# Kernel optimization log

Hardware: AMD Instinct MI355X
Metric: run time of the kernel (lower is better)

Reference implementation:

```python
import jax, jax.numpy as jnp
import numpy as np

MODEL_DIM = 512
INNER_DIM = 4 * MODEL_DIM
NUM_EXPERTS = 4
LN_EPS = 1e-5


def setup_inputs() -> dict:
    key = jax.random.key(0)
    ks = jax.random.split(key, 8)
    B, T, D, E = 8, 8192, MODEL_DIM, NUM_EXPERTS
    x = jax.random.normal(ks[0], (B, T, D), dtype=jnp.float32)
    router_prob = jax.random.uniform(ks[1], (B, T, E), dtype=jnp.float32)
    alpha = jnp.ones((), dtype=jnp.float32)
    # params (kaiming-uniform-ish init, values just need to be realistic)
    bound1 = 1.0 / np.sqrt(D)
    l1_w = jax.random.uniform(ks[2], (INNER_DIM, D), minval=-bound1, maxval=bound1, dtype=jnp.float32)
    l1_b = jax.random.uniform(ks[3], (INNER_DIM,), minval=-bound1, maxval=bound1, dtype=jnp.float32)
    bound2 = 1.0 / np.sqrt(INNER_DIM)
    l2_w = jax.random.uniform(ks[4], (D, INNER_DIM), minval=-bound2, maxval=bound2, dtype=jnp.float32)
    l2_b = jax.random.uniform(ks[5], (D,), minval=-bound2, maxval=bound2, dtype=jnp.float32)
    ln_w = jnp.ones((D,), dtype=jnp.float32)
    ln_b = jnp.zeros((D,), dtype=jnp.float32)
    return {"x": x, "router_prob": router_prob, "alpha": alpha,
            "ln_w": ln_w, "ln_b": ln_b,
            "l1_w": l1_w, "l1_b": l1_b, "l2_w": l2_w, "l2_b": l2_b}


def _layernorm(x, w, b):
    mu = jnp.mean(x, axis=-1, keepdims=True)
    var = jnp.var(x, axis=-1, keepdims=True)
    return (x - mu) * jax.lax.rsqrt(var + LN_EPS) * w + b


def reference(x, router_prob, alpha, ln_w, ln_b, l1_w, l1_b, l2_w, l2_b):
    B, T, D = x.shape
    E = router_prob.shape[-1]
    k = T // E
    brange = jnp.arange(B)[:, None]  # [B,1] for batched scatter
    rp = router_prob  # working copy; selected tokens get zeroed
    outs, probs = [], []
    for e in range(E):
        # top-k tokens for this expert among the not-yet-taken tokens
        _, idx = jax.lax.top_k(rp[:, :, e], k)          # idx: [B,k]
        xi = jnp.take_along_axis(x, idx[:, :, None], axis=1)            # [B,k,D]
        sp = jnp.take_along_axis(router_prob, idx[:, :, None], axis=1)  # [B,k,E]
        rp = rp.at[brange, idx, :].set(0.0)  # mark tokens as consumed
        # nested-width expert MLP
        xn = _layernorm(xi, ln_w, ln_b)
        m = D // (2 ** e)
        h = jax.nn.gelu(jnp.einsum('bkm,im->bki', xn[:, :, :m], l1_w[:, :m]) + l1_b,
                        approximate=False)                               # [B,k,INNER]
        o = jnp.einsum('bki,mi->bkm', h, l2_w[:m]) + l2_b[:m]            # [B,k,m]
        o = jnp.pad(o, ((0, 0), (0, 0), (0, D - m)))                     # pad back to D
        scale = alpha * sp[:, :, e:e + 1] + 1.0                          # [B,k,1]
        outs.append(xi + scale * o)
        probs.append(sp)
    final_outs = jnp.concatenate(outs, axis=1)   # [B,T,D]
    final_probs = jnp.concatenate(probs, axis=1) # [B,T,E]
    return final_outs, final_probs
```

## Files before the change

### kernel.cpp

```cpp
#include <hip/hip_runtime.h>
#include <hip/hip_bf16.h>

typedef __attribute__((ext_vector_type(8))) short  bf16x8;
typedef __attribute__((ext_vector_type(4))) short  s16x4;
typedef __attribute__((ext_vector_type(4))) float  f32x4;
typedef unsigned long long u64;

#define B_   8
#define T_   8192
#define D_   512
#define E_   4
#define INNER_ 2048
#define M_TOK 16384

static __device__ __forceinline__ short f2bf(float f) {
    union { float f; unsigned int u; } a; a.f = f;
    unsigned int u = a.u;
    u += 0x7FFFu + ((u >> 16) & 1u);
    return (short)(u >> 16);
}

static __device__ __forceinline__ void cswap(u64& a, u64& b, bool desc) {
    if (desc ? (a < b) : (a > b)) { u64 t = a; a = b; b = t; }
}

__global__ __launch_bounds__(256) void convertw(const float* __restrict__ w1,
                                                const float* __restrict__ w2,
                                                short* __restrict__ o1,
                                                short* __restrict__ o2) {
    int i = (blockIdx.x * 256 + threadIdx.x) * 4;
    if (i < 1048576) {
        float4 a = *(const float4*)(w1 + i);
        s16x4 ra; ra.x = f2bf(a.x); ra.y = f2bf(a.y); ra.z = f2bf(a.z); ra.w = f2bf(a.w);
        *(s16x4*)(o1 + i) = ra;
        float4 b = *(const float4*)(w2 + i);
        s16x4 rb; rb.x = f2bf(b.x); rb.y = f2bf(b.y); rb.z = f2bf(b.z); rb.w = f2bf(b.w);
        *(s16x4*)(o2 + i) = rb;
    }
}

__global__ __launch_bounds__(1024) void sort_kernel(const float* __restrict__ rp,
                                                    u64* __restrict__ sorted) {
    __shared__ u64 keys[8192];
    const int t = threadIdx.x;
    const int b = blockIdx.x >> 2, e = blockIdx.x & 3;
    const size_t base = (size_t)b * T_;

    u64 k[8];
    #pragma unroll
    for (int j = 0; j < 8; ++j) {
        int i = (t << 3) + j;
        float v = rp[(base + i) * E_ + e];
        unsigned vb; __builtin_memcpy(&vb, &v, 4);
        k[j] = (((u64)(vb + 1u)) << 13) | (u64)(8191 - i);
    }
    cswap(k[0], k[1], true);  cswap(k[2], k[3], false);
    cswap(k[4], k[5], true);  cswap(k[6], k[7], false);
    cswap(k[0], k[2], true);  cswap(k[1], k[3], true);
    cswap(k[4], k[6], false); cswap(k[5], k[7], false);
    cswap(k[0], k[1], true);  cswap(k[2], k[3], true);
    cswap(k[4], k[5], false); cswap(k[6], k[7], false);
    {
        bool d8 = ((t & 1) == 0);
        cswap(k[0], k[4], d8); cswap(k[1], k[5], d8); cswap(k[2], k[6], d8); cswap(k[3], k[7], d8);
        cswap(k[0], k[2], d8); cswap(k[1], k[3], d8); cswap(k[4], k[6], d8); cswap(k[5], k[7], d8);
        cswap(k[0], k[1], d8); cswap(k[2], k[3], d8); cswap(k[4], k[5], d8); cswap(k[6], k[7], d8);
    }
    #pragma unroll
    for (int j = 0; j < 8; ++j) keys[(t << 3) + j] = k[j];

    for (int size = 16; size <= 8192; size <<= 1) {
        for (int stride = size >> 1; stride >= 8; stride >>= 1) {
            __syncthreads();
            #pragma unroll
            for (int q = 0; q < 4; ++q) {
                int p = (q << 10) + t;
                int i = ((p & ~(stride - 1)) << 1) | (p & (stride - 1));
                int l = i | stride;
                bool desc = ((i & size) == 0);
                u64 a = keys[i], c = keys[l];
                if (desc ? (a < c) : (a > c)) { keys[i] = c; keys[l] = a; }
            }
        }
        __syncthreads();
        #pragma unroll
        for (int j = 0; j < 8; ++j) k[j] = keys[(t << 3) + j];
        bool d = (((t << 3) & size) == 0);
        cswap(k[0], k[4], d); cswap(k[1], k[5], d); cswap(k[2], k[6], d); cswap(k[3], k[7], d);
        cswap(k[0], k[2], d); cswap(k[1], k[3], d); cswap(k[4], k[6], d); cswap(k[5], k[7], d);
        cswap(k[0], k[1], d); cswap(k[2], k[3], d); cswap(k[4], k[5], d); cswap(k[6], k[7], d);
        #pragma unroll
        for (int j = 0; j < 8; ++j) keys[(t << 3) + j] = k[j];
    }
    __syncthreads();
    u64* dst = sorted + ((size_t)blockIdx.x << 13);
    #pragma unroll
    for (int j = 0; j < 8; ++j) {
        int i = (j << 10) + t;
        dst[i] = keys[i];
    }
}

__global__ __launch_bounds__(1024) void select_kernel(const float* __restrict__ rp,
                                                      const u64* __restrict__ sorted,
                                                      const float* __restrict__ alphaPtr,
                                                      int* __restrict__ perm,
                                                      float* __restrict__ scaleArr,
                                                      float* __restrict__ out_probs) {
    __shared__ unsigned char cons[8192];
    __shared__ int wsum[16];
    __shared__ int woff[16];
    const int t = threadIdx.x, b = blockIdx.x;
    const int lane = t & 63, wv = t >> 6;
    const size_t base = (size_t)b * T_;
    const float alphaV = *alphaPtr;

    #pragma unroll
    for (int j = 0; j < 8; ++j) cons[(t << 3) + j] = 0;
    __syncthreads();

    for (int e = 0; e < E_; ++e) {
        const u64* sk = sorted + (((size_t)(b << 2) + e) << 13);
        u64 k[8]; int idx[8]; int f[8];
        int s = 0;
        #pragma unroll
        for (int j = 0; j < 8; ++j) {
            k[j] = sk[(t << 3) + j];
            idx[j] = 8191 - (int)(k[j] & 8191ull);
            f[j] = cons[idx[j]] ? 0 : 1;
            s += f[j];
        }
        int inc = s;
        #pragma unroll
        for (int o = 1; o < 64; o <<= 1) {
            int v = __shfl_up(inc, o, 64);
            if (lane >= o) inc += v;
        }
        if (lane == 63) wsum[wv] = inc;
        __syncthreads();
        if (t == 0) {
            int acc = 0;
            for (int w = 0; w < 16; ++w) { int v = wsum[w]; woff[w] = acc; acc += v; }
        }
        __syncthreads();
        int off = woff[wv] + (inc - s);
        #pragma unroll
        for (int j = 0; j < 8; ++j) {
            if (f[j] && off < 2048) {
                int rank = off;
                unsigned vb = (unsigned)(k[j] >> 13) - 1u;
                float v; __builtin_memcpy(&v, &vb, 4);
                int rpos = (e << 14) + (b << 11) + rank;
                perm[rpos] = idx[j];
                scaleArr[rpos] = alphaV * v + 1.0f;
                size_t g = ((size_t)b << 13) + (e << 11) + rank;
                float4 pr = *(const float4*)(rp + ((base + idx[j]) << 2));
                *(float4*)(out_probs + (g << 2)) = pr;
                cons[idx[j]] = 1;
            }
            off += f[j];
        }
        __syncthreads();
    }
}

__global__ __launch_bounds__(256) void gather_ln(const float* __restrict__ x,
                                                 const int* __restrict__ perm,
                                                 const float* __restrict__ ln_w,
                                                 const float* __restrict__ ln_b,
                                                 short* __restrict__ xn,
                                                 float* __restrict__ out_outs) {
    const int wv = threadIdx.x >> 6, lane = threadIdx.x & 63;
    const int rp_ = (blockIdx.x << 2) + wv;
    const int e = rp_ >> 14, rem = rp_ & 16383, b = rem >> 11, rank = rem & 2047;
    const int idx = perm[rp_];
    const float* xr = x + (((size_t)b << 13) + idx) * D_;
    const int d0 = lane << 3;
    float4 v0 = *(const float4*)(xr + d0);
    float4 v1 = *(const float4*)(xr + d0 + 4);

    float s = v0.x + v0.y + v0.z + v0.w + v1.x + v1.y + v1.z + v1.w;
    #pragma unroll
    for (int o = 32; o > 0; o >>= 1) s += __shfl_xor(s, o, 64);
    float mu = s * (1.0f / 512.0f);

    float a0 = v0.x - mu, a1 = v0.y - mu, a2 = v0.z - mu, a3 = v0.w - mu;
    float a4 = v1.x - mu, a5 = v1.y - mu, a6 = v1.z - mu, a7 = v1.w - mu;
    float q = a0*a0 + a1*a1 + a2*a2 + a3*a3 + a4*a4 + a5*a5 + a6*a6 + a7*a7;
    #pragma unroll
    for (int o = 32; o > 0; o >>= 1) q += __shfl_xor(q, o, 64);
    float rstd = rsqrtf(q * (1.0f / 512.0f) + 1e-5f);

    const size_t g = ((size_t)b << 13) + (e << 11) + rank;
    float* op = out_outs + g * D_ + d0;
    *(float4*)op       = v0;
    *(float4*)(op + 4) = v1;

    float4 w0 = *(const float4*)(ln_w + d0);
    float4 w1 = *(const float4*)(ln_w + d0 + 4);
    float4 bb0 = *(const float4*)(ln_b + d0);
    float4 bb1 = *(const float4*)(ln_b + d0 + 4);
    bf16x8 hv;
    hv[0] = f2bf(a0 * rstd * w0.x + bb0.x);
    hv[1] = f2bf(a1 * rstd * w0.y + bb0.y);
    hv[2] = f2bf(a2 * rstd * w0.z + bb0.z);
    hv[3] = f2bf(a3 * rstd * w0.w + bb0.w);
    hv[4] = f2bf(a4 * rstd * w1.x + bb1.x);
    hv[5] = f2bf(a5 * rstd * w1.y + bb1.y);
    hv[6] = f2bf(a6 * rstd * w1.z + bb1.z);
    hv[7] = f2bf(a7 * rstd * w1.w + bb1.w);
    *(bf16x8*)(xn + (size_t)rp_ * D_ + d0) = hv;
}

template <int MODE>
__global__ __launch_bounds__(256) void gemm_bt(const short* __restrict__ A,
                                               const short* __restrict__ B,
                                               int N, int K, int lda, int ldb,
                                               const float* __restrict__ bias,
                                               short* __restrict__ H,
                                               float* __restrict__ Out,
                                               const float* __restrict__ scaleArr,
                                               int expert) {
    __shared__ short As[128 * 64];
    __shared__ short Bs[128 * 64];
    const int t = threadIdx.x;
    const int tile_n = blockIdx.x << 7;
    const int tile_m = blockIdx.y << 7;
    const int lane = t & 63, wave = t >> 6;
    const int wm = (wave >> 1) << 6, wn = (wave & 1) << 6;
    const int lrow = lane & 15, lk = (lane >> 4) << 3;
    const int ldsRow = lane >> 3;
    const int ldsCol = (lane & 7) << 3;

    f32x4 acc[4][4];
    #pragma unroll
    for (int i = 0; i < 4; ++i)
        #pragma unroll
        for (int j = 0; j < 4; ++j)
            acc[i][j] = (f32x4){0.f, 0.f, 0.f, 0.f};

    for (int k0 = 0; k0 < K; k0 += 64) {
        #pragma unroll
        for (int q = 0; q < 4; ++q) {
            int c = (wave << 2) + q;
            const short* ga = A + (size_t)(tile_m + (c << 3) + ldsRow) * lda + k0 + ldsCol;
            __builtin_amdgcn_global_load_lds(
                (const __attribute__((address_space(1))) unsigned int*)ga,
                (__attribute__((address_space(3))) unsigned int*)(As + (c << 9)),
                16, 0, 0);
            const short* gb = B + (size_t)(tile_n + (c << 3) + ldsRow) * ldb + k0 + ldsCol;
            __builtin_amdgcn_global_load_lds(
                (const __attribute__((address_space(1))) unsigned int*)gb,
                (__attribute__((address_space(3))) unsigned int*)(Bs + (c << 9)),
                16, 0, 0);
        }
        __syncthreads();
        bf16x8 af[4][2], bfr[4][2];
        #pragma unroll
        for (int f = 0; f < 4; ++f)
            #pragma unroll
            for (int kk = 0; kk < 2; ++kk) {
                af[f][kk]  = *(const bf16x8*)(As + ((wm + (f << 4) + lrow) << 6) + (kk << 5) + lk);
                bfr[f][kk] = *(const bf16x8*)(Bs + ((wn + (f << 4) + lrow) << 6) + (kk << 5) + lk);
            }
        #pragma unroll
        for (int kk = 0; kk < 2; ++kk)
            #pragma unroll
            for (int fm = 0; fm < 4; ++fm)
                #pragma unroll
                for (int fn = 0; fn < 4; ++fn)
                    acc[fm][fn] = __builtin_amdgcn_mfma_f32_16x16x32_bf16(
                        af[fm][kk], bfr[fn][kk], acc[fm][fn], 0, 0, 0);
        __syncthreads();
    }

    #pragma unroll
    for (int fm = 0; fm < 4; ++fm) {
        #pragma unroll
        for (int fn = 0; fn < 4; ++fn) {
            #pragma unroll
            for (int j = 0; j < 4; ++j) {
                int row = tile_m + wm + (fm << 4) + ((lane >> 4) << 2) + j;
                int col = tile_n + wn + (fn << 4) + (lane & 15);
                float v = acc[fm][fn][j];
                if (MODE == 1) {
                    v += bias[col];
                    v = 0.5f * v * (1.0f + erff(v * 0.7071067811865475f));
                    H[(size_t)row * (size_t)INNER_ + col] = f2bf(v);
                } else {
                    if (col < N) {
                        int bb = row >> 11, rank = row & 2047;
                        float sc = scaleArr[(expert << 14) + row];
                        float* p = Out + (((size_t)bb << 13) + (expert << 11) + rank) * D_ + col;
                        *p += sc * (v + bias[col]);
                    }
                }
            }
        }
    }
}

extern "C" void kernel_launch(void* const* d_in, const int* in_sizes, int n_in,
                              void* d_out, int out_size, void* d_ws, size_t ws_size,
                              hipStream_t stream) {
    const float* x           = (const float*)d_in[0];
    const float* router_prob = (const float*)d_in[1];
    const float* alpha       = (const float*)d_in[2];
    const float* ln_w        = (const float*)d_in[3];
    const float* ln_b        = (const float*)d_in[4];
    const float* l1_w        = (const float*)d_in[5];
    const float* l1_b        = (const float*)d_in[6];
    const float* l2_w        = (const float*)d_in[7];
    const float* l2_b        = (const float*)d_in[8];

    float* out       = (float*)d_out;
    float* out_probs = out + (size_t)B_ * T_ * D_;

    char* ws = (char*)d_ws;
    int*   perm  = (int*)(ws);
    float* scale = (float*)(ws + (1u << 18));
    short* w1b   = (short*)(ws + (2u << 18));
    short* w2b   = (short*)(ws + (2u << 18) + (1u << 21));
    short* xn    = (short*)(ws + (2u << 18) + (2u << 21));
    short* h     = (short*)(ws + (2u << 18) + (2u << 21) + (1u << 26));
    u64*   sorted = (u64*)h;

    convertw<<<1024, 256, 0, stream>>>(l1_w, l2_w, w1b, w2b);
    sort_kernel<<<32, 1024, 0, stream>>>(router_prob, sorted);
    select_kernel<<<8, 1024, 0, stream>>>(router_prob, sorted, alpha, perm, scale, out_probs);
    gather_ln<<<16384, 256, 0, stream>>>(x, perm, ln_w, ln_b, xn, out);

    for (int e = 0; e < E_; ++e) {
        int m = D_ >> e;
        gemm_bt<1><<<dim3(INNER_ / 128, M_TOK / 128), 256, 0, stream>>>(
            xn + ((size_t)e * M_TOK) * D_, w1b, INNER_, m, D_, D_, l1_b, h,
            nullptr, nullptr, 0);
        gemm_bt<2><<<dim3((m + 127) >> 7, M_TOK / 128), 256, 0, stream>>>(
            h, w2b, m, INNER_, INNER_, INNER_, l2_b, nullptr, out, scale, e);
    }
}
```

Measured before the change: 820.5 us.

## Batch expert GEMMs via grid z, split-K second GEMM, swizzle LDS, tanh GELU

After: 812.7 us. Within noise of the previous version (-0.9%).

```diff
diff --git a/kernel.cpp b/kernel.cpp
--- a/kernel.cpp
+++ b/kernel.cpp
@@ -215,22 +215,58 @@
 template <int MODE>
 __global__ __launch_bounds__(256) void gemm_bt(const short* __restrict__ A,
                                                const short* __restrict__ B,
-                                               int N, int K, int lda, int ldb,
+                                               int lda, int ldb,
                                                const float* __restrict__ bias,
                                                short* __restrict__ H,
                                                float* __restrict__ Out,
                                                const float* __restrict__ scaleArr,
-                                               int expert) {
+                                               int expertArg, size_t hStride) {
     __shared__ short As[128 * 64];
     __shared__ short Bs[128 * 64];
     const int t = threadIdx.x;
-    const int tile_n = blockIdx.x << 7;
+    const int lane = t & 63, wave = t >> 6;
+    const int e = expertArg + blockIdx.z;
     const int tile_m = blockIdx.y << 7;
-    const int lane = t & 63, wave = t >> 6;
+
+    int tile_n, kStart, nsteps, Ncols, sp;
+    bool useAtomic;
+    const short* Abase;
+    if (MODE == 1) {
+        tile_n = blockIdx.x << 7;
+        kStart = 0;
+        nsteps = (512 >> e) >> 6;
+        Ncols  = 2048;
+        Abase  = A + (size_t)e * M_TOK * D_;
+        sp = 0; useAtomic = false;
+    } else {
+        Ncols = 512 >> e;
+        int se = e < 2 ? e : 2;
+        int splits = 1 << se;
+        int sub = blockIdx.x;
+        int nt = sub >> se;
+        sp = sub & (splits - 1);
+        tile_n = nt << 7;
+        int Kslice = 2048 >> se;
+        kStart = sp * Kslice;
+        nsteps = Kslice >> 6;
+        Abase  = A + (size_t)e * hStride;
+        useAtomic = (splits > 1);
+    }
+
+    const int srow = lane >> 3;
+    const int scol = ((lane & 7) ^ srow) << 3;
+    const short* aP[4];
+    const short* bP[4];
+    #pragma unroll
+    for (int q = 0; q < 4; ++q) {
+        int c = (wave << 2) + q;
+        aP[q] = Abase + (size_t)(tile_m + (c << 3) + srow) * lda + kStart + scol;
+        bP[q] = B     + (size_t)(tile_n + (c << 3) + srow) * ldb + kStart + scol;
+    }
+
     const int wm = (wave >> 1) << 6, wn = (wave & 1) << 6;
-    const int lrow = lane & 15, lk = (lane >> 4) << 3;
-    const int ldsRow = lane >> 3;
-    const int ldsCol = (lane & 7) << 3;
+    const int lrow = lane & 15, lt = lane >> 4;
+    const int sx = lrow & 7;
 
     f32x4 acc[4][4];
     #pragma unroll
@@ -239,20 +275,19 @@
         for (int j = 0; j < 4; ++j)
             acc[i][j] = (f32x4){0.f, 0.f, 0.f, 0.f};
 
-    for (int k0 = 0; k0 < K; k0 += 64) {
+    for (int ks = 0; ks < nsteps; ++ks) {
         #pragma unroll
         for (int q = 0; q < 4; ++q) {
             int c = (wave << 2) + q;
-            const short* ga = A + (size_t)(tile_m + (c << 3) + ldsRow) * lda + k0 + ldsCol;
             __builtin_amdgcn_global_load_lds(
-                (const __attribute__((address_space(1))) unsigned int*)ga,
+                (const __attribute__((address_space(1))) unsigned int*)aP[q],
                 (__attribute__((address_space(3))) unsigned int*)(As + (c << 9)),
                 16, 0, 0);
-            const short* gb = B + (size_t)(tile_n + (c << 3) + ldsRow) * ldb + k0 + ldsCol;
             __builtin_amdgcn_global_load_lds(
-                (const __attribute__((address_space(1))) unsigned int*)gb,
+                (const __attribute__((address_space(1))) unsigned int*)bP[q],
                 (__attribute__((address_space(3))) unsigned int*)(Bs + (c << 9)),
                 16, 0, 0);
+            aP[q] += 64; bP[q] += 64;
         }
         __syncthreads();
         bf16x8 af[4][2], bfr[4][2];
@@ -260,8 +295,9 @@
         for (int f = 0; f < 4; ++f)
             #pragma unroll
             for (int kk = 0; kk < 2; ++kk) {
-                af[f][kk]  = *(const bf16x8*)(As + ((wm + (f << 4) + lrow) << 6) + (kk << 5) + lk);
-                bfr[f][kk] = *(const bf16x8*)(Bs + ((wn + (f << 4) + lrow) << 6) + (kk << 5) + lk);
+                int slot = (kk << 2) + lt;
+                af[f][kk]  = *(const bf16x8*)(As + ((wm + (f << 4) + lrow) << 6) + ((slot ^ sx) << 3));
+                bfr[f][kk] = *(const bf16x8*)(Bs + ((wn + (f << 4) + lrow) << 6) + ((slot ^ sx) << 3));
             }
         #pragma unroll
         for (int kk = 0; kk < 2; ++kk)
@@ -280,19 +316,24 @@
         for (int fn = 0; fn < 4; ++fn) {
             #pragma unroll
             for (int j = 0; j < 4; ++j) {
-                int row = tile_m + wm + (fm << 4) + ((lane >> 4) << 2) + j;
+                int row = tile_m + wm + (fm << 4) + (lt << 2) + j;
                 int col = tile_n + wn + (fn << 4) + (lane & 15);
                 float v = acc[fm][fn][j];
                 if (MODE == 1) {
                     v += bias[col];
-                    v = 0.5f * v * (1.0f + erff(v * 0.7071067811865475f));
-                    H[(size_t)row * (size_t)INNER_ + col] = f2bf(v);
+                    float u = 1.5957691216f * v * (1.0f + 0.044715f * v * v);
+                    u = fminf(u, 60.0f);
+                    float p = __expf(u);
+                    float g = v * p * __builtin_amdgcn_rcpf(p + 1.0f);
+                    (H + (size_t)e * hStride)[(size_t)row * (size_t)INNER_ + col] = f2bf(g);
                 } else {
-                    if (col < N) {
+                    if (col < Ncols) {
                         int bb = row >> 11, rank = row & 2047;
-                        float sc = scaleArr[(expert << 14) + row];
-                        float* p = Out + (((size_t)bb << 13) + (expert << 11) + rank) * D_ + col;
-                        *p += sc * (v + bias[col]);
+                        float sc = scaleArr[(e << 14) + row];
+                        float val = sc * v + (sp == 0 ? sc * bias[col] : 0.0f);
+                        float* p = Out + (((size_t)bb << 13) + (e << 11) + rank) * D_ + col;
+                        if (useAtomic) atomicAdd(p, val);
+                        else           *p += val;
                     }
                 }
             }
@@ -322,20 +363,30 @@
     short* w1b   = (short*)(ws + (2u << 18));
     short* w2b   = (short*)(ws + (2u << 18) + (1u << 21));
     short* xn    = (short*)(ws + (2u << 18) + (2u << 21));
-    short* h     = (short*)(ws + (2u << 18) + (2u << 21) + (1u << 26));
+    const size_t hOff = (size_t)(2u << 18) + (2u << 21) + (1u << 26);
+    short* h     = (short*)(ws + hOff);
     u64*   sorted = (u64*)h;
+
+    const size_t hPerExpert = (size_t)M_TOK * INNER_;
+    const bool fused = ws_size >= hOff + 4 * hPerExpert * sizeof(short);
+    const size_t hStride = fused ? hPerExpert : 0;
 
     convertw<<<1024, 256, 0, stream>>>(l1_w, l2_w, w1b, w2b);
     sort_kernel<<<32, 1024, 0, stream>>>(router_prob, sorted);
     select_kernel<<<8, 1024, 0, stream>>>(router_prob, sorted, alpha, perm, scale, out_probs);
     gather_ln<<<16384, 256, 0, stream>>>(x, perm, ln_w, ln_b, xn, out);
 
-    for (int e = 0; e < E_; ++e) {
-        int m = D_ >> e;
-        gemm_bt<1><<<dim3(INNER_ / 128, M_TOK / 128), 256, 0, stream>>>(
-            xn + ((size_t)e * M_TOK) * D_, w1b, INNER_, m, D_, D_, l1_b, h,
-            nullptr, nullptr, 0);
-        gemm_bt<2><<<dim3((m + 127) >> 7, M_TOK / 128), 256, 0, stream>>>(
-            h, w2b, m, INNER_, INNER_, INNER_, l2_b, nullptr, out, scale, e);
-    }
-}
+    if (fused) {
+        gemm_bt<1><<<dim3(16, 128, 4), 256, 0, stream>>>(
+            xn, w1b, D_, D_, l1_b, h, nullptr, nullptr, 0, hStride);
+        gemm_bt<2><<<dim3(4, 128, 4), 256, 0, stream>>>(
+            h, w2b, INNER_, INNER_, l2_b, nullptr, out, scale, 0, hStride);
+    } else {
+        for (int e = 0; e < E_; ++e) {
+            gemm_bt<1><<<dim3(16, 128, 1), 256, 0, stream>>>(
+                xn, w1b, D_, D_, l1_b, h, nullptr, nullptr, e, 0);
+            gemm_bt<2><<<dim3(4, 128, 1), 256, 0, stream>>>(
+                h, w2b, INNER_, INNER_, l2_b, nullptr, out, scale, e, 0);
+        }
+    }
+}
```
